# Performance work log

Hardware: AMD Instinct MI355X
Metric: run time of the kernel (lower is better)

## Reference

```python
import jax, jax.numpy as jnp
import numpy as np

V = 23
C_IN = 256
C_OUT = 256
N = 16384
BN_EPS = 1e-5


def _make_shift(c, sign):
    # shift_in:  idx[i*c+j] = (i*c + j + j*c) % (c*V)
    # shift_out: idx[i*c+j] = (i*c + j - j*c) % (c*V)
    i = np.arange(V)[:, None]
    j = np.arange(c)[None, :]
    idx = (i * c + j + sign * j * c) % (c * V)
    return jnp.asarray(idx.reshape(-1), dtype=jnp.int32)


def setup_inputs() -> dict:
    key = jax.random.key(0)
    k1, k2, k3 = jax.random.split(key, 3)
    x0 = jax.random.normal(k1, (N, C_IN, V), dtype=jnp.float32)
    # Linear_weight ~ N(0, sqrt(1/out_channels))
    W = jax.random.normal(k2, (C_IN, C_OUT), dtype=jnp.float32) * np.sqrt(1.0 / C_OUT)
    bias = jnp.zeros((1, 1, C_OUT), dtype=jnp.float32)
    # Feature_Mask param (init 0 in original; randomized for a non-trivial baseline)
    mask = jax.random.normal(k3, (1, V, C_IN), dtype=jnp.float32) * 0.1
    bn_weight = jnp.ones((V * C_OUT,), dtype=jnp.float32)
    bn_bias = jnp.zeros((V * C_OUT,), dtype=jnp.float32)
    shift_in = _make_shift(C_IN, +1)
    shift_out = _make_shift(C_OUT, -1)
    return {"x0": x0, "W": W, "bias": bias, "mask": mask,
            "bn_weight": bn_weight, "bn_bias": bn_bias,
            "shift_in": shift_in, "shift_out": shift_out}


def reference(x0, W, bias, mask, bn_weight, bn_bias, shift_in, shift_out):
    n, c, v = x0.shape
    c_out = W.shape[1]
    # (n, c, v) -> (n, v*c), channel-shift gather
    x = jnp.transpose(x0, (0, 2, 1)).reshape(n, v * c)
    x = x[:, shift_in]                       # gather along feature dim
    x = x.reshape(n, v, c)
    x = x * (jnp.tanh(mask) + 1.0)           # learned soft mask
    x = jnp.einsum('nwc,cd->nwd', x, W) + bias
    x = x.reshape(n, v * c_out)
    x = x[:, shift_out]                      # shift-back gather
    # BatchNorm1d over v*c_out features, training-mode batch stats (biased var)
    mean = jnp.mean(x, axis=0)
    var = jnp.var(x, axis=0)
    x = (x - mean) * jax.lax.rsqrt(var + BN_EPS) * bn_weight + bn_bias
    x = x.reshape(n, v, c_out).transpose(0, 2, 1)
    # in_channels == out_channels -> down is identity
    x = x + x0
    return jax.nn.relu(x)
```

## Files before the change

### kernel.cpp

```cpp
#include <hip/hip_runtime.h>
#include <hip/hip_bf16.h>

#define NV 23
#define NTOT 16384
#define FLAT (NV * 256)
#define FLAT4 (FLAT / 4)
#define NB 32
#define CH 184
#define NS 3
#define SLAB 23552
#define ROFF 32768
#define OOFF 103424

typedef short s16x8 __attribute__((ext_vector_type(8)));
typedef float f32x4 __attribute__((ext_vector_type(4)));
typedef unsigned u32x4 __attribute__((ext_vector_type(4)));

__device__ __forceinline__ int divNV(int x) { return (int)(((unsigned)x * 45591u) >> 20); }
__device__ __forceinline__ unsigned f2bf(float f) {
  unsigned u = __float_as_uint(f);
  u += 0x7fffu + ((u >> 16) & 1u);
  return u >> 16;
}

__device__ __forceinline__ void gl_lds16(const void* g, void* l) {
  __builtin_amdgcn_global_load_lds(
      (const __attribute__((address_space(1))) unsigned*)(unsigned long long)(uintptr_t)g,
      (__attribute__((address_space(3))) unsigned*)(unsigned)(uintptr_t)l, 16, 0, 0);
}

__global__ void k_prep(const float* __restrict__ W, const float* __restrict__ mask,
                       short* __restrict__ Wt, unsigned* __restrict__ tab,
                       float* __restrict__ sums) {
  int idx = blockIdx.x * 256 + threadIdx.x;
  int d = idx >> 8, c = idx & 255;
  Wt[idx] = (short)f2bf(W[c * 256 + d]);
  if (idx < FLAT) {
    int cc = divNV(idx);
    int v = idx - NV * cc;
    int cm = cc - NV * divNV(cc);
    int w = v - cm; w += (w >> 31) & NV;
    unsigned off = (unsigned)((w << 9) + ((cc << 1) ^ ((w & 7) << 4)));
    tab[idx] = (f2bf(tanhf(mask[(w << 8) + cc]) + 1.0f) << 16) | off;
  }
  if (idx < 2 * FLAT) sums[idx] = 0.0f;
}

__global__ void k_finalize(const float* __restrict__ sum, const float* __restrict__ ssq,
                           const float* __restrict__ bnw, const float* __restrict__ bnb,
                           float* __restrict__ An2, float* __restrict__ Bn2) {
  int idx = blockIdx.x * 256 + threadIdx.x;
  if (idx >= FLAT) return;
  int w = idx >> 8, d = idx & 255;
  float mean = sum[idx] * (1.0f / NTOT);
  float var  = ssq[idx] * (1.0f / NTOT) - mean * mean;
  float inv  = rsqrtf(var + 1e-5f);
  int i = w + d; i -= NV * divNV(i);
  float a = inv * bnw[i * 256 + d];
  An2[d * NV + i] = a;
  Bn2[d * NV + i] = bnb[i * 256 + d] - mean * a;
}

template <int WRITE>
__global__ __launch_bounds__(512) void k_gemm(
    const float* __restrict__ x0, const short* __restrict__ Wt,
    const unsigned* __restrict__ tab, float* __restrict__ sum, float* __restrict__ ssq,
    const float* __restrict__ An2, const float* __restrict__ Bn2,
    float* __restrict__ out) {
  __shared__ char smem[WRITE ? 126976 : 103424];
  float* O = (float*)(smem + OOFF);

  const int tid = threadIdx.x;
  const int lane = tid & 63;
  const int wv = tid >> 6;
  const int l15 = lane & 15;
  const int lg = lane >> 4;
  const int d0 = wv * 32;
  const int ch0 = wv * CH;

  s16x8 bfr[2][8];
#pragma unroll
  for (int nt = 0; nt < 2; ++nt)
#pragma unroll
    for (int kt = 0; kt < 8; ++kt)
      bfr[nt][kt] = *(const s16x8*)(Wt + (d0 + nt * 16 + l15) * 256 + kt * 32 + lg * 8);

  u32x4 tbr[NS];
#pragma unroll
  for (int s = 0; s < NS; ++s)
    if (s * 64 + lane < CH) tbr[s] = *(const u32x4*)(tab + 4 * (ch0 + s * 64 + lane));

  f32x4 anr[NS], bnr[NS];
  if (WRITE) {
#pragma unroll
    for (int s = 0; s < NS; ++s)
      if (s * 64 + lane < CH) {
        anr[s] = *(const f32x4*)(An2 + 4 * (ch0 + s * 64 + lane));
        bnr[s] = *(const f32x4*)(Bn2 + 4 * (ch0 + s * 64 + lane));
      }
  }

  for (int i = tid; i < 2304; i += 512) {
    int b = i >= 1152;
    *(int*)(smem + b * 16384 + 11776 + (i - b * 1152) * 4) = 0;
  }

  float s1[2][2][4], s2[2][2][4];
  if (!WRITE) {
#pragma unroll
    for (int mt = 0; mt < 2; ++mt)
#pragma unroll
      for (int nt = 0; nt < 2; ++nt)
#pragma unroll
        for (int r = 0; r < 4; ++r) { s1[mt][nt][r] = 0.f; s2[mt][nt][r] = 0.f; }
  }

  const int nbase = blockIdx.x * NB;
  auto nmap = [&](int T) { return nbase + (WRITE ? (NB - 1 - T) : T); };

  auto stage = [&](int T) {
    if (T >= NB) return;
    const char* gs = (const char*)(x0 + (size_t)nmap(T) * FLAT);
    char* lb = smem + ROFF + (T % 3) * SLAB;
    gl_lds16(gs + (wv << 10) + lane * 16, lb + (wv << 10));
    gl_lds16(gs + ((8 + wv) << 10) + lane * 16, lb + ((8 + wv) << 10));
    if (wv < 7)
      gl_lds16(gs + ((16 + wv) << 10) + lane * 16, lb + ((16 + wv) << 10));
  };
  auto form = [&](int T) {
    if (T >= NB) return;
    const char* rb = smem + ROFF + (T % 3) * SLAB;
    char* xb = smem + (T & 1) * 16384;
#pragma unroll
    for (int s = 0; s < NS; ++s)
      if (s * 64 + lane < CH) {
        f32x4 xv = *(const f32x4*)(rb + (ch0 + s * 64 + lane) * 16);
        u32x4 tb = tbr[s];
#pragma unroll
        for (int e = 0; e < 4; ++e) {
          unsigned tt = tb[e];
          *(short*)(xb + (tt & 0xffffu)) =
              (short)f2bf(xv[e] * __uint_as_float(tt & 0xffff0000u));
        }
      }
  };
  auto bar = []() {
    asm volatile("s_waitcnt lgkmcnt(0)" ::: "memory");
    __builtin_amdgcn_s_barrier();
    asm volatile("" ::: "memory");
  };

  stage(0);
  stage(1);
  asm volatile("s_waitcnt vmcnt(0)" ::: "memory");
  bar();
  form(0);

  for (int t = 0; t < NB; ++t) {
    if (WRITE && t) asm volatile("s_waitcnt vmcnt(3)" ::: "memory");
    else            asm volatile("s_waitcnt vmcnt(0)" ::: "memory");
    bar();
    stage(t + 2);
    form(t + 1);

    const char* xb = smem + (t & 1) * 16384;
    f32x4 acc[2][2];
#pragma unroll
    for (int mt = 0; mt < 2; ++mt)
#pragma unroll
      for (int nt = 0; nt < 2; ++nt) acc[mt][nt] = (f32x4){0.f, 0.f, 0.f, 0.f};
#pragma unroll
    for (int kt = 0; kt < 8; ++kt) {
      s16x8 af[2];
#pragma unroll
      for (int mt = 0; mt < 2; ++mt) {
        int row = mt * 16 + l15;
        af[mt] = *(const s16x8*)(xb + (row << 9) +
                                 (((kt * 32 + lg * 8) << 1) ^ ((row & 7) << 4)));
      }
#pragma unroll
      for (int mt = 0; mt < 2; ++mt)
#pragma unroll
        for (int nt = 0; nt < 2; ++nt)
          acc[mt][nt] = __builtin_amdgcn_mfma_f32_16x16x32_bf16(
              af[mt], bfr[nt][kt], acc[mt][nt], 0, 0, 0);
    }

    if (!WRITE) {
#pragma unroll
      for (int mt = 0; mt < 2; ++mt)
#pragma unroll
        for (int nt = 0; nt < 2; ++nt)
#pragma unroll
          for (int r = 0; r < 4; ++r) {
            float y = acc[mt][nt][r];
            s1[mt][nt][r] += y;
            s2[mt][nt][r] += y * y;
          }
    } else {
#pragma unroll
      for (int mt = 0; mt < 2; ++mt)
#pragma unroll
        for (int nt = 0; nt < 2; ++nt)
#pragma unroll
          for (int r = 0; r < 4; ++r) {
            int w = mt * 16 + lg * 4 + r;
            if (w < NV) {
              int d = d0 + nt * 16 + l15;
              int sj = w + d; sj -= NV * divNV(sj);
              O[d * NV + sj] = acc[mt][nt][r];
            }
          }
      const char* rb = smem + ROFF + (t % 3) * SLAB;
      float* og = out + (size_t)nmap(t) * FLAT;
#pragma unroll
      for (int s = 0; s < NS; ++s)
        if (s * 64 + lane < CH) {
          int i = ch0 + s * 64 + lane;
          f32x4 y = *(const f32x4*)(O + 4 * i);
          f32x4 sl = *(const f32x4*)(rb + i * 16);
          f32x4 o;
#pragma unroll
          for (int e = 0; e < 4; ++e)
            o[e] = fmaxf(fmaf(y[e], anr[s][e], bnr[s][e]) + sl[e], 0.0f);
          __builtin_nontemporal_store(o, (f32x4*)og + i);
        }
    }
  }

  if (!WRITE) {
#pragma unroll
    for (int mt = 0; mt < 2; ++mt)
#pragma unroll
      for (int nt = 0; nt < 2; ++nt)
#pragma unroll
        for (int r = 0; r < 4; ++r) {
          int w = mt * 16 + lg * 4 + r;
          if (w < NV) {
            int d = d0 + nt * 16 + l15;
            atomicAdd(sum + (w << 8) + d, s1[mt][nt][r]);
            atomicAdd(ssq + (w << 8) + d, s2[mt][nt][r]);
          }
        }
  }
}

extern "C" void kernel_launch(void* const* d_in, const int* in_sizes, int n_in,
                              void* d_out, int out_size, void* d_ws, size_t ws_size,
                              hipStream_t stream) {
  const float* x0   = (const float*)d_in[0];
  const float* W    = (const float*)d_in[1];
  const float* mask = (const float*)d_in[3];
  const float* bnw  = (const float*)d_in[4];
  const float* bnb  = (const float*)d_in[5];
  float* out = (float*)d_out;

  char* ws = (char*)d_ws;
  short* Wt     = (short*)ws;
  unsigned* tab = (unsigned*)(ws + 131072);
  float* sum    = (float*)(ws + 154624);
  float* ssq    = (float*)(ws + 178176);
  float* An2    = (float*)(ws + 201728);
  float* Bn2    = (float*)(ws + 225280);

  k_prep<<<256, 256, 0, stream>>>(W, mask, Wt, tab, sum);
  k_gemm<0><<<512, 512, 0, stream>>>(x0, Wt, tab, sum, ssq, nullptr, nullptr, nullptr);
  k_finalize<<<23, 256, 0, stream>>>(sum, ssq, bnw, bnb, An2, Bn2);
  k_gemm<1><<<512, 512, 0, stream>>>(x0, Wt, tab, sum, ssq, An2, Bn2, out);
}
```

Measured before the change: 280.1 us.

## Deepen stats-pass pipeline to two tiles per barrier with larger blocks and new swizzle

The statistics pass now processes 64 samples per block on 256 blocks. It uses four raw and four bf16 LDS buffers so each barrier covers two tiles, staging two ahead and forming two ahead. The LDS XOR swizzle changes to a new per-row function meant to cut bank conflicts on A-fragment reads. MFMA sections are wrapped in s_setprio. The cost is higher LDS use (about 156KB) in the stats kernel and half as many blocks, which may hurt occupancy and load balance across CUs.

```diff
diff --git a/kernel.cpp b/kernel.cpp
--- a/kernel.cpp
+++ b/kernel.cpp
@@ -5,12 +5,15 @@
 #define NTOT 16384
 #define FLAT (NV * 256)
 #define FLAT4 (FLAT / 4)
-#define NB 32
 #define CH 184
 #define NS 3
 #define SLAB 23552
-#define ROFF 32768
-#define OOFF 103424
+
+#define NB0 64
+#define ROFF0 65536
+#define NB1 32
+#define ROFF1 32768
+#define OOFF1 103424
 
 typedef short s16x8 __attribute__((ext_vector_type(8)));
 typedef float f32x4 __attribute__((ext_vector_type(4)));
@@ -22,6 +25,7 @@
   u += 0x7fffu + ((u >> 16) & 1u);
   return u >> 16;
 }
+__device__ __forceinline__ int fsw(int w) { return ((w + (w >> 3)) * 3) & 7; }
 
 __device__ __forceinline__ void gl_lds16(const void* g, void* l) {
   __builtin_amdgcn_global_load_lds(
@@ -40,7 +44,7 @@
     int v = idx - NV * cc;
     int cm = cc - NV * divNV(cc);
     int w = v - cm; w += (w >> 31) & NV;
-    unsigned off = (unsigned)((w << 9) + ((cc << 1) ^ ((w & 7) << 4)));
+    unsigned off = (unsigned)((w << 9) + ((cc << 1) ^ (fsw(w) << 4)));
     tab[idx] = (f2bf(tanhf(mask[(w << 8) + cc]) + 1.0f) << 16) | off;
   }
   if (idx < 2 * FLAT) sums[idx] = 0.0f;
@@ -67,8 +71,12 @@
     const unsigned* __restrict__ tab, float* __restrict__ sum, float* __restrict__ ssq,
     const float* __restrict__ An2, const float* __restrict__ Bn2,
     float* __restrict__ out) {
-  __shared__ char smem[WRITE ? 126976 : 103424];
-  float* O = (float*)(smem + OOFF);
+  __shared__ char smem[WRITE ? 126976 : 159744];
+  constexpr int ROFF = WRITE ? ROFF1 : ROFF0;
+  constexpr int NXB = WRITE ? 2 : 4;
+  constexpr int NRB = WRITE ? 3 : 4;
+  constexpr int NB  = WRITE ? NB1 : NB0;
+  float* O = (float*)(smem + OOFF1);
 
   const int tid = threadIdx.x;
   const int lane = tid & 63;
@@ -77,6 +85,8 @@
   const int lg = lane >> 4;
   const int d0 = wv * 32;
   const int ch0 = wv * CH;
+  const int fr0 = fsw(l15) << 4;
+  const int fr1 = fsw(16 + l15) << 4;
 
   s16x8 bfr[2][8];
 #pragma unroll
@@ -100,8 +110,8 @@
       }
   }
 
-  for (int i = tid; i < 2304; i += 512) {
-    int b = i >= 1152;
+  for (int i = tid; i < NXB * 1152; i += 512) {
+    int b = i / 1152;
     *(int*)(smem + b * 16384 + 11776 + (i - b * 1152) * 4) = 0;
   }
 
@@ -121,7 +131,7 @@
   auto stage = [&](int T) {
     if (T >= NB) return;
     const char* gs = (const char*)(x0 + (size_t)nmap(T) * FLAT);
-    char* lb = smem + ROFF + (T % 3) * SLAB;
+    char* lb = smem + ROFF + (T % NRB) * SLAB;
     gl_lds16(gs + (wv << 10) + lane * 16, lb + (wv << 10));
     gl_lds16(gs + ((8 + wv) << 10) + lane * 16, lb + ((8 + wv) << 10));
     if (wv < 7)
@@ -129,8 +139,8 @@
   };
   auto form = [&](int T) {
     if (T >= NB) return;
-    const char* rb = smem + ROFF + (T % 3) * SLAB;
-    char* xb = smem + (T & 1) * 16384;
+    const char* rb = smem + ROFF + (T % NRB) * SLAB;
+    char* xb = smem + (T % NXB) * 16384;
 #pragma unroll
     for (int s = 0; s < NS; ++s)
       if (s * 64 + lane < CH) {
@@ -144,91 +154,66 @@
         }
       }
   };
+  auto mstep = [&](int T, f32x4 (*acc)[2]) {
+    const char* xb = smem + (T % NXB) * 16384;
+#pragma unroll
+    for (int kt = 0; kt < 8; ++kt) {
+      s16x8 af[2];
+      af[0] = *(const s16x8*)(xb + (l15 << 9) + ((kt * 64 + lg * 16) ^ fr0));
+      af[1] = *(const s16x8*)(xb + ((16 + l15) << 9) + ((kt * 64 + lg * 16) ^ fr1));
+#pragma unroll
+      for (int mt = 0; mt < 2; ++mt)
+#pragma unroll
+        for (int nt = 0; nt < 2; ++nt)
+          acc[mt][nt] = __builtin_amdgcn_mfma_f32_16x16x32_bf16(
+              af[mt], bfr[nt][kt], acc[mt][nt], 0, 0, 0);
+    }
+  };
+  auto sstep = [&](f32x4 (*acc)[2]) {
+#pragma unroll
+    for (int mt = 0; mt < 2; ++mt)
+#pragma unroll
+      for (int nt = 0; nt < 2; ++nt)
+#pragma unroll
+        for (int r = 0; r < 4; ++r) {
+          float y = acc[mt][nt][r];
+          s1[mt][nt][r] += y;
+          s2[mt][nt][r] += y * y;
+        }
+  };
   auto bar = []() {
     asm volatile("s_waitcnt lgkmcnt(0)" ::: "memory");
     __builtin_amdgcn_s_barrier();
     asm volatile("" ::: "memory");
   };
 
-  stage(0);
-  stage(1);
-  asm volatile("s_waitcnt vmcnt(0)" ::: "memory");
-  bar();
-  form(0);
-
-  for (int t = 0; t < NB; ++t) {
-    if (WRITE && t) asm volatile("s_waitcnt vmcnt(3)" ::: "memory");
-    else            asm volatile("s_waitcnt vmcnt(0)" ::: "memory");
+  if (!WRITE) {
+    stage(0); stage(1); stage(2); stage(3);
+    asm volatile("s_waitcnt vmcnt(0)" ::: "memory");
     bar();
-    stage(t + 2);
-    form(t + 1);
-
-    const char* xb = smem + (t & 1) * 16384;
-    f32x4 acc[2][2];
-#pragma unroll
-    for (int mt = 0; mt < 2; ++mt)
-#pragma unroll
-      for (int nt = 0; nt < 2; ++nt) acc[mt][nt] = (f32x4){0.f, 0.f, 0.f, 0.f};
-#pragma unroll
-    for (int kt = 0; kt < 8; ++kt) {
-      s16x8 af[2];
-#pragma unroll
-      for (int mt = 0; mt < 2; ++mt) {
-        int row = mt * 16 + l15;
-        af[mt] = *(const s16x8*)(xb + (row << 9) +
-                                 (((kt * 32 + lg * 8) << 1) ^ ((row & 7) << 4)));
-      }
+    form(0); form(1);
+    for (int u = 0; u < NB0 / 2; ++u) {
+      int t = 2 * u;
+      asm volatile("s_waitcnt vmcnt(0)" ::: "memory");
+      bar();
+      stage(t + 4); stage(t + 5);
+      form(t + 2); form(t + 3);
+      f32x4 acc[2][2];
+      __builtin_amdgcn_s_setprio(1);
 #pragma unroll
       for (int mt = 0; mt < 2; ++mt)
 #pragma unroll
-        for (int nt = 0; nt < 2; ++nt)
-          acc[mt][nt] = __builtin_amdgcn_mfma_f32_16x16x32_bf16(
-              af[mt], bfr[nt][kt], acc[mt][nt], 0, 0, 0);
+        for (int nt = 0; nt < 2; ++nt) acc[mt][nt] = (f32x4){0.f, 0.f, 0.f, 0.f};
+      mstep(t, acc);
+      sstep(acc);
+#pragma unroll
+      for (int mt = 0; mt < 2; ++mt)
+#pragma unroll
+        for (int nt = 0; nt < 2; ++nt) acc[mt][nt] = (f32x4){0.f, 0.f, 0.f, 0.f};
+      mstep(t + 1, acc);
+      __builtin_amdgcn_s_setprio(0);
+      sstep(acc);
     }
-
-    if (!WRITE) {
-#pragma unroll
-      for (int mt = 0; mt < 2; ++mt)
-#pragma unroll
-        for (int nt = 0; nt < 2; ++nt)
-#pragma unroll
-          for (int r = 0; r < 4; ++r) {
-            float y = acc[mt][nt][r];
-            s1[mt][nt][r] += y;
-            s2[mt][nt][r] += y * y;
-          }
-    } else {
-#pragma unroll
-      for (int mt = 0; mt < 2; ++mt)
-#pragma unroll
-        for (int nt = 0; nt < 2; ++nt)
-#pragma unroll
-          for (int r = 0; r < 4; ++r) {
-            int w = mt * 16 + lg * 4 + r;
-            if (w < NV) {
-              int d = d0 + nt * 16 + l15;
-              int sj = w + d; sj -= NV * divNV(sj);
-              O[d * NV + sj] = acc[mt][nt][r];
-            }
-          }
-      const char* rb = smem + ROFF + (t % 3) * SLAB;
-      float* og = out + (size_t)nmap(t) * FLAT;
-#pragma unroll
-      for (int s = 0; s < NS; ++s)
-        if (s * 64 + lane < CH) {
-          int i = ch0 + s * 64 + lane;
-          f32x4 y = *(const f32x4*)(O + 4 * i);
-          f32x4 sl = *(const f32x4*)(rb + i * 16);
-          f32x4 o;
-#pragma unroll
-          for (int e = 0; e < 4; ++e)
-            o[e] = fmaxf(fmaf(y[e], anr[s][e], bnr[s][e]) + sl[e], 0.0f);
-          __builtin_nontemporal_store(o, (f32x4*)og + i);
-        }
-    }
-  }
-
-  if (!WRITE) {
 #pragma unroll
     for (int mt = 0; mt < 2; ++mt)
 #pragma unroll
@@ -242,6 +227,57 @@
             atomicAdd(ssq + (w << 8) + d, s2[mt][nt][r]);
           }
         }
+    return;
+  }
+
+  stage(0); stage(1);
+  asm volatile("s_waitcnt vmcnt(0)" ::: "memory");
+  bar();
+  form(0);
+
+  for (int t = 0; t < NB1; ++t) {
+    if (t) asm volatile("s_waitcnt vmcnt(3)" ::: "memory");
+    else   asm volatile("s_waitcnt vmcnt(0)" ::: "memory");
+    bar();
+    stage(t + 2);
+    form(t + 1);
+
+    f32x4 acc[2][2];
+#pragma unroll
+    for (int mt = 0; mt < 2; ++mt)
+#pragma unroll
+      for (int nt = 0; nt < 2; ++nt) acc[mt][nt] = (f32x4){0.f, 0.f, 0.f, 0.f};
+    __builtin_amdgcn_s_setprio(1);
+    mstep(t, acc);
+    __builtin_amdgcn_s_setprio(0);
+
+#pragma unroll
+    for (int mt = 0; mt < 2; ++mt)
+#pragma unroll
+      for (int nt = 0; nt < 2; ++nt)
+#pragma unroll
+        for (int r = 0; r < 4; ++r) {
+          int w = mt * 16 + lg * 4 + r;
+          if (w < NV) {
+            int d = d0 + nt * 16 + l15;
+            int sj = w + d; sj -= NV * divNV(sj);
+            O[d * NV + sj] = acc[mt][nt][r];
+          }
+        }
+    const char* rb = smem + ROFF + (t % NRB) * SLAB;
+    float* og = out + (size_t)nmap(t) * FLAT;
+#pragma unroll
+    for (int s = 0; s < NS; ++s)
+      if (s * 64 + lane < CH) {
+        int i = ch0 + s * 64 + lane;
+        f32x4 y = *(const f32x4*)(O + 4 * i);
+        f32x4 sl = *(const f32x4*)(rb + i * 16);
+        f32x4 o;
+#pragma unroll
+        for (int e = 0; e < 4; ++e)
+          o[e] = fmaxf(fmaf(y[e], anr[s][e], bnr[s][e]) + sl[e], 0.0f);
+        __builtin_nontemporal_store(o, (f32x4*)og + i);
+      }
   }
 }
 
@@ -264,7 +300,7 @@
   float* Bn2    = (float*)(ws + 225280);
 
   k_prep<<<256, 256, 0, stream>>>(W, mask, Wt, tab, sum);
-  k_gemm<0><<<512, 512, 0, stream>>>(x0, Wt, tab, sum, ssq, nullptr, nullptr, nullptr);
+  k_gemm<0><<<256, 512, 0, stream>>>(x0, Wt, tab, sum, ssq, nullptr, nullptr, nullptr);
   k_finalize<<<23, 256, 0, stream>>>(sum, ssq, bnw, bnb, An2, Bn2);
   k_gemm<1><<<512, 512, 0, stream>>>(x0, Wt, tab, sum, ssq, An2, Bn2, out);
 }
```

Result: no change. 277.8 us (-0.8%).
